# Optimization experiments

Measured on AMD Instinct MI355X. Metric: run time of the kernel, lower is better.

The kernel has to match this reference:

```python
import jax, jax.numpy as jnp
import numpy as np
import math

B, S, H = 8, 1024, 1024
LN_EPS = 1e-5  # assumed epsilon of create_normalization_layer('layer_norm')


def setup_inputs() -> dict:
    key = jax.random.key(0)
    ks = jax.random.split(key, 6)
    context = jax.random.normal(ks[0], (B, S, H), dtype=jnp.float32)
    mask = jnp.ones((B, 1, S), dtype=jnp.int32)
    prior = jax.random.uniform(ks[1], (B, S, S), dtype=jnp.float32)
    # LayerNorm params
    gamma = jnp.ones((H,), dtype=jnp.float32)
    beta = jnp.zeros((H,), dtype=jnp.float32)
    # Dense projections (Glorot-like init)
    scale = 1.0 / np.sqrt(H)
    Wk = jax.random.normal(ks[2], (H, H), dtype=jnp.float32) * scale
    bk = jnp.zeros((H,), dtype=jnp.float32)
    Wq = jax.random.normal(ks[3], (H, H), dtype=jnp.float32) * scale
    bq = jnp.zeros((H,), dtype=jnp.float32)
    return {"context": context, "mask": mask, "prior": prior,
            "gamma": gamma, "beta": beta, "Wk": Wk, "bk": bk, "Wq": Wq, "bq": bq}


def reference(context, mask, prior, gamma, beta, Wk, bk, Wq, bq):
    dtype = context.dtype
    s = context.shape[1]
    hs = context.shape[2]
    i = jnp.arange(s)
    adj_upper = i[:, None] == (i[None, :] - 1)          # [S,S] superdiagonal
    adj_lower = i[:, None] == (i[None, :] + 1)          # subdiagonal
    adj_mask = adj_upper | adj_lower
    pad = mask[:, 0, :].astype(bool)                    # [B,S]
    pad2d = pad[:, :, None] & pad[:, None, :]           # [B,S,S]
    final_adj = adj_mask[None, :, :] & pad2d

    # LayerNorm over last axis
    mu = jnp.mean(context, axis=-1, keepdims=True)
    var = jnp.mean(jnp.square(context - mu), axis=-1, keepdims=True)
    cn = (context - mu) * jax.lax.rsqrt(var + LN_EPS) * gamma + beta

    k = cn @ Wk + bk                                    # [B,S,H]
    q = cn @ Wq + bq
    scores = jnp.einsum('bsh,bth->bst', q, k) / math.sqrt(hs)
    scores = jnp.where(final_adj, scores, jnp.asarray(-1e9, dtype))
    neibor = jax.nn.softmax(scores, axis=-1)
    neibor = jnp.sqrt(neibor * jnp.swapaxes(neibor, 1, 2) + 1e-9)
    neibor = prior + (1.0 - prior) * neibor

    triu = i[None, :] >= i[:, None]                     # [S,S] upper incl diag
    tri = triu.astype(dtype)
    b_eye = jnp.eye(s, dtype=bool)

    t = jnp.log(neibor + 1e-9)
    t = jnp.where(adj_upper[None, :, :], t, jnp.asarray(0.0, dtype))
    t = jnp.einsum('bij,jk->bik', t, tri)               # cumulative over cols
    g = jnp.exp(jnp.einsum('ij,bjk->bik', tri, t))      # hierarchical prefix product
    keep = jnp.logical_not(jnp.logical_xor(triu, b_eye))
    g = jnp.where(keep[None, :, :], g, jnp.asarray(0.0, dtype))
    neibor_diag = jnp.where(b_eye[None, :, :], jnp.asarray(1e-9, dtype), neibor)
    g = g + jnp.swapaxes(g, 1, 2) + neibor_diag
    g = g / (jnp.sum(g, axis=-1, keepdims=True) + 1e-9)

    f2d = pad2d.astype(dtype)
    g = g * f2d
    neibor = neibor * f2d
    return g, neibor
```

## Files before the change

kernel.cpp:

```cpp
#include <hip/hip_runtime.h>
#include <hip/hip_bf16.h>

#define SB 8
#define SS 1024
#define SH 1024
#define LN_EPS 1e-5f

typedef unsigned short u16;
typedef __attribute__((ext_vector_type(8))) short bf16x8;
typedef __attribute__((ext_vector_type(4))) float f32x4;

__device__ __forceinline__ u16 f2bf(float f) {
  __hip_bfloat16 h = __float2bfloat16(f);
  return *reinterpret_cast<u16*>(&h);
}
__device__ __forceinline__ float bf2f(u16 x) {
  unsigned v = ((unsigned)x) << 16;
  return __builtin_bit_cast(float, v);
}
__device__ __forceinline__ ushort4 pack4(float a, float b, float c, float d) {
  ushort4 o;
  o.x = f2bf(a); o.y = f2bf(b); o.z = f2bf(c); o.w = f2bf(d);
  return o;
}

__device__ __forceinline__ void gld16(const void* g, void* l) {
  __builtin_amdgcn_global_load_lds(
      (const __attribute__((address_space(1))) void*)g,
      (__attribute__((address_space(3))) void*)l, 16, 0, 0);
}

#define NPT 256
#define NWB 16
#define LNB0 (NPT + NWB)

__global__ __launch_bounds__(256) void prep_pt(
    const float* __restrict__ x, const float* __restrict__ gamma,
    const float* __restrict__ beta, const float* __restrict__ Wq,
    const float* __restrict__ Wk, const float* __restrict__ bq,
    u16* __restrict__ cnb, u16* __restrict__ PT, float* __restrict__ wkbq,
    float* __restrict__ du, float* __restrict__ dd) {
  __shared__ float p1[4], p2[4];
  __shared__ u16 As[64 * 32];
  __shared__ u16 Bs[64 * 32];
  const int blk = blockIdx.x;
  const int t = threadIdx.x;
  const int wave = t >> 6, lane = t & 63;

  if (blk >= LNB0) {
    const int row = blk - LNB0;
    const float* xr = x + (size_t)row * SH;
    float4 v = *(const float4*)(xr + 4 * t);

    float s = v.x + v.y + v.z + v.w;
#pragma unroll
    for (int off = 32; off > 0; off >>= 1) s += __shfl_down(s, off, 64);
    if (lane == 0) p1[wave] = s;
    __syncthreads();
    const float mu = (p1[0] + p1[1] + p1[2] + p1[3]) * (1.0f / SH);

    float d0 = v.x - mu, d1 = v.y - mu, d2 = v.z - mu, d3 = v.w - mu;
    float ss = d0 * d0 + d1 * d1 + d2 * d2 + d3 * d3;
#pragma unroll
    for (int off = 32; off > 0; off >>= 1) ss += __shfl_down(ss, off, 64);
    if (lane == 0) p2[wave] = ss;
    __syncthreads();
    const float rstd =
        rsqrtf((p2[0] + p2[1] + p2[2] + p2[3]) * (1.0f / SH) + LN_EPS);

    float4 gm = *(const float4*)(gamma + 4 * t);
    float4 bt = *(const float4*)(beta + 4 * t);
    ushort4 o = pack4(d0 * rstd * gm.x + bt.x, d1 * rstd * gm.y + bt.y,
                      d2 * rstd * gm.z + bt.z, d3 * rstd * gm.w + bt.w);
    *(ushort4*)(cnb + (size_t)row * SH + 4 * t) = o;
    if (t == 0) {
      du[row] = 0.f;
      dd[row] = 0.f;
    }
  } else if (blk < NPT) {
    const int m0 = (blk >> 4) * 64;
    const int n0 = (blk & 15) * 64;
    const int wn = wave * 16;
    const int l15 = lane & 15, q = lane >> 4;

    f32x4 acc[4] = {};

    const int srow = t >> 2;
    const int scol = (t & 3) * 8;
    const float* gA = Wk + (size_t)(m0 + srow) * SH + scol;
    const float* gB = Wq + (size_t)(n0 + srow) * SH + scol;
    u16* lA = &As[srow * 32 + scol];
    u16* lB = &Bs[srow * 32 + scol];

    for (int k0 = 0; k0 < SH; k0 += 32) {
      float4 a0 = *(const float4*)(gA + k0);
      float4 a1 = *(const float4*)(gA + k0 + 4);
      float4 b0 = *(const float4*)(gB + k0);
      float4 b1 = *(const float4*)(gB + k0 + 4);
      __syncthreads();
      *(ushort4*)lA = pack4(a0.x, a0.y, a0.z, a0.w);
      *(ushort4*)(lA + 4) = pack4(a1.x, a1.y, a1.z, a1.w);
      *(ushort4*)lB = pack4(b0.x, b0.y, b0.z, b0.w);
      *(ushort4*)(lB + 4) = pack4(b1.x, b1.y, b1.z, b1.w);
      __syncthreads();

      bf16x8 af[4];
#pragma unroll
      for (int fm = 0; fm < 4; ++fm)
        af[fm] = *(const bf16x8*)&As[(fm * 16 + l15) * 32 + q * 8];
      bf16x8 bfr = *(const bf16x8*)&Bs[(wn + l15) * 32 + q * 8];
#pragma unroll
      for (int fm = 0; fm < 4; ++fm)
        acc[fm] = __builtin_amdgcn_mfma_f32_16x16x32_bf16(af[fm], bfr, acc[fm],
                                                          0, 0, 0);
    }

#pragma unroll
    for (int fm = 0; fm < 4; ++fm) {
      const int row0 = m0 + fm * 16 + q * 4;
      const int col = n0 + wn + l15;
#pragma unroll
      for (int r = 0; r < 4; ++r)
        PT[(size_t)(row0 + r) * SH + col] = f2bf(acc[fm][r]);
    }
  } else {
    const int rbase = (blk - NPT) * 64 + wave * 16;
    float4 bv[4];
#pragma unroll
    for (int j = 0; j < 4; ++j)
      bv[j] = *(const float4*)(bq + lane * 16 + 4 * j);
    for (int i = 0; i < 16; ++i) {
      const float* wr = Wk + (size_t)(rbase + i) * SH + lane * 16;
      float s = 0.f;
#pragma unroll
      for (int j = 0; j < 4; ++j) {
        float4 w4 = *(const float4*)(wr + 4 * j);
        s += w4.x * bv[j].x + w4.y * bv[j].y + w4.z * bv[j].z + w4.w * bv[j].w;
      }
#pragma unroll
      for (int off = 32; off > 0; off >>= 1) s += __shfl_down(s, off, 64);
      if (lane == 0) wkbq[rbase + i] = s;
    }
  }
}

#define GK 1024
#define GN 1024
#define BM 128
#define BN 128
#define BK 32

__global__ __launch_bounds__(256) void ugemm_fused(const u16* __restrict__ A,
                                                   const u16* __restrict__ Bt,
                                                   const u16* __restrict__ cnb,
                                                   const float* __restrict__ wkbq,
                                                   float* __restrict__ du,
                                                   float* __restrict__ dd) {
  __shared__ u16 As[BM * BK];
  __shared__ u16 Bs[BN * BK];
  __shared__ u16 cn_s[144 * 128];
  const int tid = threadIdx.x;
  const int m0 = blockIdx.y * BM;
  const int n0 = blockIdx.x * BN;
  const int wave = tid >> 6, lane = tid & 63;
  const int wm = (wave & 1) * 64, wn = (wave >> 1) * 64;
  const int l15 = lane & 15, q = lane >> 4;

  {
    const int lr4 = lane >> 4;
    const int cb = lane & 15;
#pragma unroll
    for (int rd = 0; rd < 9; ++rd) {
      const int rowbase = rd * 16 + wave * 4;
      const int rowi = rowbase + lr4;
      const int sw = (rowi >> 2) & 3;
      int gr = m0 - 1 + rowi;
      gr = max(0, min(SB * SS - 1, gr));
      gld16(cnb + (size_t)gr * SH + n0 + (((cb ^ (sw << 1))) << 3),
            &cn_s[rowbase * 128]);
    }
  }

  f32x4 acc[4][4] = {};

  const int srow = tid >> 2;
  const int scol = 8 * (tid & 3);
  const u16* gA = A + (size_t)(m0 + srow) * GK + scol;
  const u16* gB = Bt + (size_t)(n0 + srow) * GK + scol;
  u16* lA = &As[srow * BK + scol];
  u16* lB = &Bs[srow * BK + scol];

  for (int k0 = 0; k0 < GK; k0 += BK) {
    __syncthreads();
    gld16(gA + k0, lA);
    gld16(gA + (size_t)64 * GK + k0, lA + 64 * BK);
    gld16(gB + k0, lB);
    gld16(gB + (size_t)64 * GK + k0, lB + 64 * BK);
    __syncthreads();

    bf16x8 af[4], bfr[4];
#pragma unroll
    for (int fm = 0; fm < 4; ++fm)
      af[fm] = *(const bf16x8*)&As[(wm + fm * 16 + l15) * BK + q * 8];
#pragma unroll
    for (int fn = 0; fn < 4; ++fn)
      bfr[fn] = *(const bf16x8*)&Bs[(wn + fn * 16 + l15) * BK + q * 8];
#pragma unroll
    for (int fm = 0; fm < 4; ++fm)
#pragma unroll
      for (int fn = 0; fn < 4; ++fn)
        acc[fm][fn] = __builtin_amdgcn_mfma_f32_16x16x32_bf16(
            af[fm], bfr[fn], acc[fm][fn], 0, 0, 0);
  }

  float wb[4];
#pragma unroll
  for (int fn = 0; fn < 4; ++fn) wb[fn] = wkbq[n0 + wn + fn * 16 + l15];

#pragma unroll
  for (int fm = 0; fm < 4; ++fm) {
#pragma unroll
    for (int rr = 0; rr < 4; ++rr) {
      const int lr = wm + fm * 16 + q * 4 + rr;
      const int r = m0 + lr;
      const int sl = r & (SS - 1);
      const int ru = lr + 2;
      const int swu = ((ru >> 2) & 3) << 4;
      const int swd = ((lr >> 2) & 3) << 4;
      const u16* up = &cn_s[ru * 128];
      const u16* dn = &cn_s[lr * 128];
      float sdu = 0.f, sdd = 0.f;
#pragma unroll
      for (int fn = 0; fn < 4; ++fn) {
        const int lc = wn + fn * 16 + l15;
        const float a = acc[fm][fn][rr] + wb[fn];
        sdu += a * bf2f(up[lc ^ swu]);
        sdd += a * bf2f(dn[lc ^ swd]);
      }
      if (sl == SS - 1) sdu = 0.f;
      if (sl == 0) sdd = 0.f;
#pragma unroll
      for (int m = 1; m < 16; m <<= 1) {
        sdu += __shfl_xor(sdu, m, 64);
        sdd += __shfl_xor(sdd, m, 64);
      }
      if (l15 == 0) {
        atomicAdd(&du[r], sdu);
        atomicAdd(&dd[r], sdd);
      }
    }
  }
}

__device__ __forceinline__ void soft2(const float* __restrict__ du,
                                      const float* __restrict__ dd, int x,
                                      float& pu, float& pd) {
  const int sl = x & (SS - 1);
  if (sl == 0) { pu = 1.f; pd = 0.f; }
  else if (sl == SS - 1) { pu = 0.f; pd = 1.f; }
  else {
    const float a = du[x] * 0.03125f;
    const float b = dd[x] * 0.03125f;
    const float m = fmaxf(a, b);
    const float eu = __expf(a - m), ed = __expf(b - m);
    const float inv = 1.f / (eu + ed);
    pu = eu * inv;
    pd = ed * inv;
  }
}

__global__ __launch_bounds__(256) void rows_fused(const float* __restrict__ prior,
                                                  const int* __restrict__ mask,
                                                  const float* __restrict__ du,
                                                  const float* __restrict__ dd,
                                                  float* __restrict__ g_out,
                                                  float* __restrict__ ne_out) {
  const int r = blockIdx.x;
  const int b = r >> 10, i = r & (SS - 1);
  const int t = threadIdx.x;
  const int wave = t >> 6, lane = t & 63;
  const float nbz = 3.1622776601683795e-5f;

  float nb_im1 = nbz, nb_ip1 = nbz;
  if (i >= 1) {
    float pu_m, pd_m, pu_c, pd_c;
    soft2(du, dd, r - 1, pu_m, pd_m);
    soft2(du, dd, r, pu_c, pd_c);
    nb_im1 = sqrtf(pu_m * pd_c + 1e-9f);
  }
  if (i <= SS - 2) {
    float pu_c, pd_c, pu_p, pd_p;
    soft2(du, dd, r, pu_c, pd_c);
    soft2(du, dd, r + 1, pu_p, pd_p);
    nb_ip1 = sqrtf(pu_c * pd_p + 1e-9f);
  }

  const float* prow = prior + (size_t)r * SS;
  float4 pr = *(const float4*)(prow + 4 * t);
  const int* mrow = mask + b * SS;
  const float padi = (mrow[i] != 0) ? 1.f : 0.f;
  int4 mk = *(const int4*)(mrow + 4 * t);

  float ne[4], gsum = 0.f;
#pragma unroll
  for (int v = 0; v < 4; ++v) {
    const int k = 4 * t + v;
    const float p = (&pr.x)[v];
    const float nb = (k == i - 1) ? nb_im1 : (k == i + 1) ? nb_ip1 : nbz;
    const float n = p + (1.f - p) * nb;
    ne[v] = n;
    gsum += (k == i) ? (2.f + 1e-9f) : (1.f + n);
  }

  __shared__ float part[4];
#pragma unroll
  for (int off = 32; off > 0; off >>= 1) gsum += __shfl_down(gsum, off, 64);
  if (lane == 0) part[wave] = gsum;
  __syncthreads();
  const float inv = 1.f / (part[0] + part[1] + part[2] + part[3] + 1e-9f);

  float4 go, no;
#pragma unroll
  for (int v = 0; v < 4; ++v) {
    const int k = 4 * t + v;
    const float padk = ((&mk.x)[v] != 0) ? 1.f : 0.f;
    const float f2 = padi * padk;
    const float gt = (k == i) ? (2.f + 1e-9f) : (1.f + ne[v]);
    (&go.x)[v] = gt * inv * f2;
    (&no.x)[v] = ne[v] * f2;
  }
  *(float4*)(g_out + (size_t)r * SS + 4 * t) = go;
  *(float4*)(ne_out + (size_t)r * SS + 4 * t) = no;
}

extern "C" void kernel_launch(void* const* d_in, const int* in_sizes, int n_in,
                              void* d_out, int out_size, void* d_ws, size_t ws_size,
                              hipStream_t stream) {
  const float* context = (const float*)d_in[0];
  const int* mask = (const int*)d_in[1];
  const float* prior = (const float*)d_in[2];
  const float* gamma = (const float*)d_in[3];
  const float* beta = (const float*)d_in[4];
  const float* Wk = (const float*)d_in[5];
  const float* bk = (const float*)d_in[6];
  const float* Wq = (const float*)d_in[7];
  const float* bq = (const float*)d_in[8];
  (void)bk;

  float* out_g = (float*)d_out;
  float* out_n = out_g + (size_t)SB * SS * SS;

  char* ws = (char*)d_ws;
  u16* cnb = (u16*)ws;
  u16* PT = (u16*)(ws + ((size_t)16 << 20));
  float* wkbq = (float*)(ws + ((size_t)18 << 20));
  float* du = (float*)(ws + ((size_t)19 << 20));
  float* dd = (float*)(ws + ((size_t)20 << 20));

  prep_pt<<<LNB0 + SB * SS, 256, 0, stream>>>(context, gamma, beta, Wq, Wk, bq,
                                              cnb, PT, wkbq, du, dd);
  ugemm_fused<<<dim3(8, 64), 256, 0, stream>>>(cnb, PT, cnb, wkbq, du, dd);
  rows_fused<<<SB * SS, 256, 0, stream>>>(prior, mask, du, dd, out_g, out_n);
}
```

Measured before the change: 191.5 us.

## Merge three kernels into one cooperative persistent kernel with grid syncs

Replaces the prep, GEMM and row-output kernels with a single cooperative kernel of 512 blocks that separates the phases with grid.sync(). LayerNorm rows are spread across all blocks after the small weight GEMM, and the row output phase has each block loop over 16 rows. The aim is to remove launch gaps and tail effects between kernels. In exchange, grid-wide barriers are added, occupancy is capped at two blocks per CU, and the memory-bound final phase runs with far fewer blocks, which may lower bandwidth utilisation.

```diff
diff --git a/kernel.cpp b/kernel.cpp
--- a/kernel.cpp
+++ b/kernel.cpp
@@ -1,11 +1,19 @@
 #include <hip/hip_runtime.h>
 #include <hip/hip_bf16.h>
+#include <hip/hip_cooperative_groups.h>
+
+namespace cg = cooperative_groups;
 
 #define SB 8
 #define SS 1024
 #define SH 1024
 #define LN_EPS 1e-5f
 
+#define GK 1024
+#define BM 128
+#define BN 128
+#define BK 32
+
 typedef unsigned short u16;
 typedef __attribute__((ext_vector_type(8))) short bf16x8;
 typedef __attribute__((ext_vector_type(4))) float f32x4;
@@ -23,233 +31,10 @@
   o.x = f2bf(a); o.y = f2bf(b); o.z = f2bf(c); o.w = f2bf(d);
   return o;
 }
-
 __device__ __forceinline__ void gld16(const void* g, void* l) {
   __builtin_amdgcn_global_load_lds(
       (const __attribute__((address_space(1))) void*)g,
       (__attribute__((address_space(3))) void*)l, 16, 0, 0);
-}
-
-#define NPT 256
-#define NWB 16
-#define LNB0 (NPT + NWB)
-
-__global__ __launch_bounds__(256) void prep_pt(
-    const float* __restrict__ x, const float* __restrict__ gamma,
-    const float* __restrict__ beta, const float* __restrict__ Wq,
-    const float* __restrict__ Wk, const float* __restrict__ bq,
-    u16* __restrict__ cnb, u16* __restrict__ PT, float* __restrict__ wkbq,
-    float* __restrict__ du, float* __restrict__ dd) {
-  __shared__ float p1[4], p2[4];
-  __shared__ u16 As[64 * 32];
-  __shared__ u16 Bs[64 * 32];
-  const int blk = blockIdx.x;
-  const int t = threadIdx.x;
-  const int wave = t >> 6, lane = t & 63;
-
-  if (blk >= LNB0) {
-    const int row = blk - LNB0;
-    const float* xr = x + (size_t)row * SH;
-    float4 v = *(const float4*)(xr + 4 * t);
-
-    float s = v.x + v.y + v.z + v.w;
-#pragma unroll
-    for (int off = 32; off > 0; off >>= 1) s += __shfl_down(s, off, 64);
-    if (lane == 0) p1[wave] = s;
-    __syncthreads();
-    const float mu = (p1[0] + p1[1] + p1[2] + p1[3]) * (1.0f / SH);
-
-    float d0 = v.x - mu, d1 = v.y - mu, d2 = v.z - mu, d3 = v.w - mu;
-    float ss = d0 * d0 + d1 * d1 + d2 * d2 + d3 * d3;
-#pragma unroll
-    for (int off = 32; off > 0; off >>= 1) ss += __shfl_down(ss, off, 64);
-    if (lane == 0) p2[wave] = ss;
-    __syncthreads();
-    const float rstd =
-        rsqrtf((p2[0] + p2[1] + p2[2] + p2[3]) * (1.0f / SH) + LN_EPS);
-
-    float4 gm = *(const float4*)(gamma + 4 * t);
-    float4 bt = *(const float4*)(beta + 4 * t);
-    ushort4 o = pack4(d0 * rstd * gm.x + bt.x, d1 * rstd * gm.y + bt.y,
-                      d2 * rstd * gm.z + bt.z, d3 * rstd * gm.w + bt.w);
-    *(ushort4*)(cnb + (size_t)row * SH + 4 * t) = o;
-    if (t == 0) {
-      du[row] = 0.f;
-      dd[row] = 0.f;
-    }
-  } else if (blk < NPT) {
-    const int m0 = (blk >> 4) * 64;
-    const int n0 = (blk & 15) * 64;
-    const int wn = wave * 16;
-    const int l15 = lane & 15, q = lane >> 4;
-
-    f32x4 acc[4] = {};
-
-    const int srow = t >> 2;
-    const int scol = (t & 3) * 8;
-    const float* gA = Wk + (size_t)(m0 + srow) * SH + scol;
-    const float* gB = Wq + (size_t)(n0 + srow) * SH + scol;
-    u16* lA = &As[srow * 32 + scol];
-    u16* lB = &Bs[srow * 32 + scol];
-
-    for (int k0 = 0; k0 < SH; k0 += 32) {
-      float4 a0 = *(const float4*)(gA + k0);
-      float4 a1 = *(const float4*)(gA + k0 + 4);
-      float4 b0 = *(const float4*)(gB + k0);
-      float4 b1 = *(const float4*)(gB + k0 + 4);
-      __syncthreads();
-      *(ushort4*)lA = pack4(a0.x, a0.y, a0.z, a0.w);
-      *(ushort4*)(lA + 4) = pack4(a1.x, a1.y, a1.z, a1.w);
-      *(ushort4*)lB = pack4(b0.x, b0.y, b0.z, b0.w);
-      *(ushort4*)(lB + 4) = pack4(b1.x, b1.y, b1.z, b1.w);
-      __syncthreads();
-
-      bf16x8 af[4];
-#pragma unroll
-      for (int fm = 0; fm < 4; ++fm)
-        af[fm] = *(const bf16x8*)&As[(fm * 16 + l15) * 32 + q * 8];
-      bf16x8 bfr = *(const bf16x8*)&Bs[(wn + l15) * 32 + q * 8];
-#pragma unroll
-      for (int fm = 0; fm < 4; ++fm)
-        acc[fm] = __builtin_amdgcn_mfma_f32_16x16x32_bf16(af[fm], bfr, acc[fm],
-                                                          0, 0, 0);
-    }
-
-#pragma unroll
-    for (int fm = 0; fm < 4; ++fm) {
-      const int row0 = m0 + fm * 16 + q * 4;
-      const int col = n0 + wn + l15;
-#pragma unroll
-      for (int r = 0; r < 4; ++r)
-        PT[(size_t)(row0 + r) * SH + col] = f2bf(acc[fm][r]);
-    }
-  } else {
-    const int rbase = (blk - NPT) * 64 + wave * 16;
-    float4 bv[4];
-#pragma unroll
-    for (int j = 0; j < 4; ++j)
-      bv[j] = *(const float4*)(bq + lane * 16 + 4 * j);
-    for (int i = 0; i < 16; ++i) {
-      const float* wr = Wk + (size_t)(rbase + i) * SH + lane * 16;
-      float s = 0.f;
-#pragma unroll
-      for (int j = 0; j < 4; ++j) {
-        float4 w4 = *(const float4*)(wr + 4 * j);
-        s += w4.x * bv[j].x + w4.y * bv[j].y + w4.z * bv[j].z + w4.w * bv[j].w;
-      }
-#pragma unroll
-      for (int off = 32; off > 0; off >>= 1) s += __shfl_down(s, off, 64);
-      if (lane == 0) wkbq[rbase + i] = s;
-    }
-  }
-}
-
-#define GK 1024
-#define GN 1024
-#define BM 128
-#define BN 128
-#define BK 32
-
-__global__ __launch_bounds__(256) void ugemm_fused(const u16* __restrict__ A,
-                                                   const u16* __restrict__ Bt,
-                                                   const u16* __restrict__ cnb,
-                                                   const float* __restrict__ wkbq,
-                                                   float* __restrict__ du,
-                                                   float* __restrict__ dd) {
-  __shared__ u16 As[BM * BK];
-  __shared__ u16 Bs[BN * BK];
-  __shared__ u16 cn_s[144 * 128];
-  const int tid = threadIdx.x;
-  const int m0 = blockIdx.y * BM;
-  const int n0 = blockIdx.x * BN;
-  const int wave = tid >> 6, lane = tid & 63;
-  const int wm = (wave & 1) * 64, wn = (wave >> 1) * 64;
-  const int l15 = lane & 15, q = lane >> 4;
-
-  {
-    const int lr4 = lane >> 4;
-    const int cb = lane & 15;
-#pragma unroll
-    for (int rd = 0; rd < 9; ++rd) {
-      const int rowbase = rd * 16 + wave * 4;
-      const int rowi = rowbase + lr4;
-      const int sw = (rowi >> 2) & 3;
-      int gr = m0 - 1 + rowi;
-      gr = max(0, min(SB * SS - 1, gr));
-      gld16(cnb + (size_t)gr * SH + n0 + (((cb ^ (sw << 1))) << 3),
-            &cn_s[rowbase * 128]);
-    }
-  }
-
-  f32x4 acc[4][4] = {};
-
-  const int srow = tid >> 2;
-  const int scol = 8 * (tid & 3);
-  const u16* gA = A + (size_t)(m0 + srow) * GK + scol;
-  const u16* gB = Bt + (size_t)(n0 + srow) * GK + scol;
-  u16* lA = &As[srow * BK + scol];
-  u16* lB = &Bs[srow * BK + scol];
-
-  for (int k0 = 0; k0 < GK; k0 += BK) {
-    __syncthreads();
-    gld16(gA + k0, lA);
-    gld16(gA + (size_t)64 * GK + k0, lA + 64 * BK);
-    gld16(gB + k0, lB);
-    gld16(gB + (size_t)64 * GK + k0, lB + 64 * BK);
-    __syncthreads();
-
-    bf16x8 af[4], bfr[4];
-#pragma unroll
-    for (int fm = 0; fm < 4; ++fm)
-      af[fm] = *(const bf16x8*)&As[(wm + fm * 16 + l15) * BK + q * 8];
-#pragma unroll
-    for (int fn = 0; fn < 4; ++fn)
-      bfr[fn] = *(const bf16x8*)&Bs[(wn + fn * 16 + l15) * BK + q * 8];
-#pragma unroll
-    for (int fm = 0; fm < 4; ++fm)
-#pragma unroll
-      for (int fn = 0; fn < 4; ++fn)
-        acc[fm][fn] = __builtin_amdgcn_mfma_f32_16x16x32_bf16(
-            af[fm], bfr[fn], acc[fm][fn], 0, 0, 0);
-  }
-
-  float wb[4];
-#pragma unroll
-  for (int fn = 0; fn < 4; ++fn) wb[fn] = wkbq[n0 + wn + fn * 16 + l15];
-
-#pragma unroll
-  for (int fm = 0; fm < 4; ++fm) {
-#pragma unroll
-    for (int rr = 0; rr < 4; ++rr) {
-      const int lr = wm + fm * 16 + q * 4 + rr;
-      const int r = m0 + lr;
-      const int sl = r & (SS - 1);
-      const int ru = lr + 2;
-      const int swu = ((ru >> 2) & 3) << 4;
-      const int swd = ((lr >> 2) & 3) << 4;
-      const u16* up = &cn_s[ru * 128];
-      const u16* dn = &cn_s[lr * 128];
-      float sdu = 0.f, sdd = 0.f;
-#pragma unroll
-      for (int fn = 0; fn < 4; ++fn) {
-        const int lc = wn + fn * 16 + l15;
-        const float a = acc[fm][fn][rr] + wb[fn];
-        sdu += a * bf2f(up[lc ^ swu]);
-        sdd += a * bf2f(dn[lc ^ swd]);
-      }
-      if (sl == SS - 1) sdu = 0.f;
-      if (sl == 0) sdd = 0.f;
-#pragma unroll
-      for (int m = 1; m < 16; m <<= 1) {
-        sdu += __shfl_xor(sdu, m, 64);
-        sdd += __shfl_xor(sdd, m, 64);
-      }
-      if (l15 == 0) {
-        atomicAdd(&du[r], sdu);
-        atomicAdd(&dd[r], sdd);
-      }
-    }
-  }
 }
 
 __device__ __forceinline__ void soft2(const float* __restrict__ du,
@@ -269,68 +54,290 @@
   }
 }
 
-__global__ __launch_bounds__(256) void rows_fused(const float* __restrict__ prior,
-                                                  const int* __restrict__ mask,
-                                                  const float* __restrict__ du,
-                                                  const float* __restrict__ dd,
-                                                  float* __restrict__ g_out,
-                                                  float* __restrict__ ne_out) {
-  const int r = blockIdx.x;
-  const int b = r >> 10, i = r & (SS - 1);
-  const int t = threadIdx.x;
-  const int wave = t >> 6, lane = t & 63;
-  const float nbz = 3.1622776601683795e-5f;
-
-  float nb_im1 = nbz, nb_ip1 = nbz;
-  if (i >= 1) {
-    float pu_m, pd_m, pu_c, pd_c;
-    soft2(du, dd, r - 1, pu_m, pd_m);
-    soft2(du, dd, r, pu_c, pd_c);
-    nb_im1 = sqrtf(pu_m * pd_c + 1e-9f);
-  }
-  if (i <= SS - 2) {
-    float pu_c, pd_c, pu_p, pd_p;
-    soft2(du, dd, r, pu_c, pd_c);
-    soft2(du, dd, r + 1, pu_p, pd_p);
-    nb_ip1 = sqrtf(pu_c * pd_p + 1e-9f);
-  }
-
-  const float* prow = prior + (size_t)r * SS;
-  float4 pr = *(const float4*)(prow + 4 * t);
-  const int* mrow = mask + b * SS;
-  const float padi = (mrow[i] != 0) ? 1.f : 0.f;
-  int4 mk = *(const int4*)(mrow + 4 * t);
-
-  float ne[4], gsum = 0.f;
-#pragma unroll
-  for (int v = 0; v < 4; ++v) {
-    const int k = 4 * t + v;
-    const float p = (&pr.x)[v];
-    const float nb = (k == i - 1) ? nb_im1 : (k == i + 1) ? nb_ip1 : nbz;
-    const float n = p + (1.f - p) * nb;
-    ne[v] = n;
-    gsum += (k == i) ? (2.f + 1e-9f) : (1.f + n);
-  }
-
-  __shared__ float part[4];
-#pragma unroll
-  for (int off = 32; off > 0; off >>= 1) gsum += __shfl_down(gsum, off, 64);
-  if (lane == 0) part[wave] = gsum;
-  __syncthreads();
-  const float inv = 1.f / (part[0] + part[1] + part[2] + part[3] + 1e-9f);
-
-  float4 go, no;
-#pragma unroll
-  for (int v = 0; v < 4; ++v) {
-    const int k = 4 * t + v;
-    const float padk = ((&mk.x)[v] != 0) ? 1.f : 0.f;
-    const float f2 = padi * padk;
-    const float gt = (k == i) ? (2.f + 1e-9f) : (1.f + ne[v]);
-    (&go.x)[v] = gt * inv * f2;
-    (&no.x)[v] = ne[v] * f2;
-  }
-  *(float4*)(g_out + (size_t)r * SS + 4 * t) = go;
-  *(float4*)(ne_out + (size_t)r * SS + 4 * t) = no;
+#define AS_OFF 0
+#define BS_OFF 8192
+#define CN_OFF 16384
+#define PR_OFF 53248
+#define SMEM_BYTES 53280
+
+__global__ __launch_bounds__(256, 2) void mega(
+    const float* __restrict__ x, const float* __restrict__ gamma,
+    const float* __restrict__ beta, const float* __restrict__ Wq,
+    const float* __restrict__ Wk, const float* __restrict__ bq,
+    const float* __restrict__ prior, const int* __restrict__ mask,
+    u16* __restrict__ cnb, u16* __restrict__ PT, float* __restrict__ wkbq,
+    float* __restrict__ du, float* __restrict__ dd,
+    float* __restrict__ g_out, float* __restrict__ ne_out) {
+  __shared__ __align__(16) char smem[SMEM_BYTES];
+  u16* As = (u16*)(smem + AS_OFF);
+  u16* Bs = (u16*)(smem + BS_OFF);
+  u16* cn_s = (u16*)(smem + CN_OFF);
+  float* p1 = (float*)(smem + PR_OFF);
+  float* p2 = p1 + 4;
+
+  const int bid = blockIdx.x;
+  const int tid = threadIdx.x;
+  const int wave = tid >> 6, lane = tid & 63;
+  cg::grid_group grid = cg::this_grid();
+
+  if (bid < 256) {
+    const int m0 = (bid >> 4) * 64;
+    const int n0 = (bid & 15) * 64;
+    const int wn = wave * 16;
+    const int l15 = lane & 15, q = lane >> 4;
+    u16* tA = As;
+    u16* tB = As + 2048;
+
+    f32x4 acc[4] = {};
+    const int srow = tid >> 2;
+    const int scol = (tid & 3) * 8;
+    const float* gA = Wk + (size_t)(m0 + srow) * SH + scol;
+    const float* gB = Wq + (size_t)(n0 + srow) * SH + scol;
+    u16* lA = &tA[srow * 32 + scol];
+    u16* lB = &tB[srow * 32 + scol];
+
+    for (int k0 = 0; k0 < SH; k0 += 32) {
+      float4 a0 = *(const float4*)(gA + k0);
+      float4 a1 = *(const float4*)(gA + k0 + 4);
+      float4 b0 = *(const float4*)(gB + k0);
+      float4 b1 = *(const float4*)(gB + k0 + 4);
+      __syncthreads();
+      *(ushort4*)lA = pack4(a0.x, a0.y, a0.z, a0.w);
+      *(ushort4*)(lA + 4) = pack4(a1.x, a1.y, a1.z, a1.w);
+      *(ushort4*)lB = pack4(b0.x, b0.y, b0.z, b0.w);
+      *(ushort4*)(lB + 4) = pack4(b1.x, b1.y, b1.z, b1.w);
+      __syncthreads();
+
+      bf16x8 af[4];
+#pragma unroll
+      for (int fm = 0; fm < 4; ++fm)
+        af[fm] = *(const bf16x8*)&tA[(fm * 16 + l15) * 32 + q * 8];
+      bf16x8 bfr = *(const bf16x8*)&tB[(wn + l15) * 32 + q * 8];
+#pragma unroll
+      for (int fm = 0; fm < 4; ++fm)
+        acc[fm] = __builtin_amdgcn_mfma_f32_16x16x32_bf16(af[fm], bfr, acc[fm],
+                                                          0, 0, 0);
+    }
+    __syncthreads();
+#pragma unroll
+    for (int fm = 0; fm < 4; ++fm) {
+      const int row0 = m0 + fm * 16 + q * 4;
+      const int col = n0 + wn + l15;
+#pragma unroll
+      for (int r = 0; r < 4; ++r)
+        PT[(size_t)(row0 + r) * SH + col] = f2bf(acc[fm][r]);
+    }
+  } else if (bid < 272) {
+    const int rbase = (bid - 256) * 64 + wave * 16;
+    float4 bv[4];
+#pragma unroll
+    for (int j = 0; j < 4; ++j)
+      bv[j] = *(const float4*)(bq + lane * 16 + 4 * j);
+    for (int i = 0; i < 16; ++i) {
+      const float* wr = Wk + (size_t)(rbase + i) * SH + lane * 16;
+      float s = 0.f;
+#pragma unroll
+      for (int j = 0; j < 4; ++j) {
+        float4 w4 = *(const float4*)(wr + 4 * j);
+        s += w4.x * bv[j].x + w4.y * bv[j].y + w4.z * bv[j].z + w4.w * bv[j].w;
+      }
+#pragma unroll
+      for (int off = 32; off > 0; off >>= 1) s += __shfl_down(s, off, 64);
+      if (lane == 0) wkbq[rbase + i] = s;
+    }
+  }
+
+  {
+    int row0, nrows;
+    if (bid < 256) { row0 = bid * 8; nrows = 8; }
+    else { row0 = 2048 + (bid - 256) * 24; nrows = 24; }
+    const float4 gm = *(const float4*)(gamma + 4 * tid);
+    const float4 bt = *(const float4*)(beta + 4 * tid);
+    for (int j = 0; j < nrows; ++j) {
+      const int row = row0 + j;
+      const float* xr = x + (size_t)row * SH;
+      float4 v = *(const float4*)(xr + 4 * tid);
+
+      float s = v.x + v.y + v.z + v.w;
+#pragma unroll
+      for (int off = 32; off > 0; off >>= 1) s += __shfl_down(s, off, 64);
+      if (lane == 0) p1[wave] = s;
+      __syncthreads();
+      const float mu = (p1[0] + p1[1] + p1[2] + p1[3]) * (1.0f / SH);
+
+      float d0 = v.x - mu, d1 = v.y - mu, d2 = v.z - mu, d3 = v.w - mu;
+      float ss = d0 * d0 + d1 * d1 + d2 * d2 + d3 * d3;
+#pragma unroll
+      for (int off = 32; off > 0; off >>= 1) ss += __shfl_down(ss, off, 64);
+      if (lane == 0) p2[wave] = ss;
+      __syncthreads();
+      const float rstd =
+          rsqrtf((p2[0] + p2[1] + p2[2] + p2[3]) * (1.0f / SH) + LN_EPS);
+
+      ushort4 o = pack4(d0 * rstd * gm.x + bt.x, d1 * rstd * gm.y + bt.y,
+                        d2 * rstd * gm.z + bt.z, d3 * rstd * gm.w + bt.w);
+      *(ushort4*)(cnb + (size_t)row * SH + 4 * tid) = o;
+      if (tid == 0) {
+        du[row] = 0.f;
+        dd[row] = 0.f;
+      }
+    }
+  }
+
+  grid.sync();
+
+  {
+    const int bx = bid & 7, by = bid >> 3;
+    const int m0 = by * BM, n0 = bx * BN;
+    const int wm = (wave & 1) * 64, wn = (wave >> 1) * 64;
+    const int l15 = lane & 15, q = lane >> 4;
+
+    {
+      const int lr4 = lane >> 4;
+      const int cb = lane & 15;
+#pragma unroll
+      for (int rd = 0; rd < 9; ++rd) {
+        const int rowbase = rd * 16 + wave * 4;
+        const int rowi = rowbase + lr4;
+        const int sw = (rowi >> 2) & 3;
+        int gr = m0 - 1 + rowi;
+        gr = max(0, min(SB * SS - 1, gr));
+        gld16(cnb + (size_t)gr * SH + n0 + ((cb ^ (sw << 1)) << 3),
+              &cn_s[rowbase * 128]);
+      }
+    }
+
+    f32x4 acc[4][4] = {};
+    const int srow = tid >> 2;
+    const int scol = 8 * (tid & 3);
+    const u16* gA = cnb + (size_t)(m0 + srow) * GK + scol;
+    const u16* gB = PT + (size_t)(n0 + srow) * GK + scol;
+    u16* lA = &As[srow * BK + scol];
+    u16* lB = &Bs[srow * BK + scol];
+
+    for (int k0 = 0; k0 < GK; k0 += BK) {
+      __syncthreads();
+      gld16(gA + k0, lA);
+      gld16(gA + (size_t)64 * GK + k0, lA + 64 * BK);
+      gld16(gB + k0, lB);
+      gld16(gB + (size_t)64 * GK + k0, lB + 64 * BK);
+      __syncthreads();
+
+      bf16x8 af[4], bfr[4];
+#pragma unroll
+      for (int fm = 0; fm < 4; ++fm)
+        af[fm] = *(const bf16x8*)&As[(wm + fm * 16 + l15) * BK + q * 8];
+#pragma unroll
+      for (int fn = 0; fn < 4; ++fn)
+        bfr[fn] = *(const bf16x8*)&Bs[(wn + fn * 16 + l15) * BK + q * 8];
+#pragma unroll
+      for (int fm = 0; fm < 4; ++fm)
+#pragma unroll
+        for (int fn = 0; fn < 4; ++fn)
+          acc[fm][fn] = __builtin_amdgcn_mfma_f32_16x16x32_bf16(
+              af[fm], bfr[fn], acc[fm][fn], 0, 0, 0);
+    }
+
+    float wb[4];
+#pragma unroll
+    for (int fn = 0; fn < 4; ++fn) wb[fn] = wkbq[n0 + wn + fn * 16 + l15];
+
+#pragma unroll
+    for (int fm = 0; fm < 4; ++fm) {
+#pragma unroll
+      for (int rr = 0; rr < 4; ++rr) {
+        const int lr = wm + fm * 16 + q * 4 + rr;
+        const int r = m0 + lr;
+        const int sl = r & (SS - 1);
+        const int ru = lr + 2;
+        const int swu = ((ru >> 2) & 3) << 4;
+        const int swd = ((lr >> 2) & 3) << 4;
+        const u16* up = &cn_s[ru * 128];
+        const u16* dn = &cn_s[lr * 128];
+        float sdu = 0.f, sdd = 0.f;
+#pragma unroll
+        for (int fn = 0; fn < 4; ++fn) {
+          const int lc = wn + fn * 16 + l15;
+          const float a = acc[fm][fn][rr] + wb[fn];
+          sdu += a * bf2f(up[lc ^ swu]);
+          sdd += a * bf2f(dn[lc ^ swd]);
+        }
+        if (sl == SS - 1) sdu = 0.f;
+        if (sl == 0) sdd = 0.f;
+#pragma unroll
+        for (int m = 1; m < 16; m <<= 1) {
+          sdu += __shfl_xor(sdu, m, 64);
+          sdd += __shfl_xor(sdd, m, 64);
+        }
+        if (l15 == 0) {
+          atomicAdd(&du[r], sdu);
+          atomicAdd(&dd[r], sdd);
+        }
+      }
+    }
+  }
+
+  grid.sync();
+
+  {
+    float* part = p1;
+    const float nbz = 3.1622776601683795e-5f;
+    for (int j = 0; j < 16; ++j) {
+      const int r = bid * 16 + j;
+      const int b = r >> 10, i = r & (SS - 1);
+
+      float nb_im1 = nbz, nb_ip1 = nbz;
+      if (i >= 1) {
+        float pu_m, pd_m, pu_c, pd_c;
+        soft2(du, dd, r - 1, pu_m, pd_m);
+        soft2(du, dd, r, pu_c, pd_c);
+        nb_im1 = sqrtf(pu_m * pd_c + 1e-9f);
+      }
+      if (i <= SS - 2) {
+        float pu_c, pd_c, pu_p, pd_p;
+        soft2(du, dd, r, pu_c, pd_c);
+        soft2(du, dd, r + 1, pu_p, pd_p);
+        nb_ip1 = sqrtf(pu_c * pd_p + 1e-9f);
+      }
+
+      const float* prow = prior + (size_t)r * SS;
+      float4 pv = *(const float4*)(prow + 4 * tid);
+      const int* mrow = mask + b * SS;
+      const float padi = (mrow[i] != 0) ? 1.f : 0.f;
+      int4 mk = *(const int4*)(mrow + 4 * tid);
+
+      float ne[4], gsum = 0.f;
+#pragma unroll
+      for (int v = 0; v < 4; ++v) {
+        const int k = 4 * tid + v;
+        const float p = (&pv.x)[v];
+        const float nb = (k == i - 1) ? nb_im1 : (k == i + 1) ? nb_ip1 : nbz;
+        const float n = p + (1.f - p) * nb;
+        ne[v] = n;
+        gsum += (k == i) ? (2.f + 1e-9f) : (1.f + n);
+      }
+
+#pragma unroll
+      for (int off = 32; off > 0; off >>= 1) gsum += __shfl_down(gsum, off, 64);
+      if (lane == 0) part[wave] = gsum;
+      __syncthreads();
+      const float inv = 1.f / (part[0] + part[1] + part[2] + part[3] + 1e-9f);
+      __syncthreads();
+
+      float4 go, no;
+#pragma unroll
+      for (int v = 0; v < 4; ++v) {
+        const int k = 4 * tid + v;
+        const float padk = ((&mk.x)[v] != 0) ? 1.f : 0.f;
+        const float f2 = padi * padk;
+        const float gt = (k == i) ? (2.f + 1e-9f) : (1.f + ne[v]);
+        (&go.x)[v] = gt * inv * f2;
+        (&no.x)[v] = ne[v] * f2;
+      }
+      *(float4*)(g_out + (size_t)r * SS + 4 * tid) = go;
+      *(float4*)(ne_out + (size_t)r * SS + 4 * tid) = no;
+    }
+  }
 }
 
 extern "C" void kernel_launch(void* const* d_in, const int* in_sizes, int n_in,
@@ -357,8 +364,10 @@
   float* du = (float*)(ws + ((size_t)19 << 20));
   float* dd = (float*)(ws + ((size_t)20 << 20));
 
-  prep_pt<<<LNB0 + SB * SS, 256, 0, stream>>>(context, gamma, beta, Wq, Wk, bq,
-                                              cnb, PT, wkbq, du, dd);
-  ugemm_fused<<<dim3(8, 64), 256, 0, stream>>>(cnb, PT, cnb, wkbq, du, dd);
-  rows_fused<<<SB * SS, 256, 0, stream>>>(prior, mask, du, dd, out_g, out_n);
-}
+  void* kargs[] = {(void*)&context, (void*)&gamma, (void*)&beta, (void*)&Wq,
+                   (void*)&Wk,      (void*)&bq,    (void*)&prior, (void*)&mask,
+                   (void*)&cnb,     (void*)&PT,    (void*)&wkbq,  (void*)&du,
+                   (void*)&dd,      (void*)&out_g, (void*)&out_n};
+  hipLaunchCooperativeKernel((void*)mega, dim3(512), dim3(256), kargs, 0,
+                             stream);
+}
```

New measurement: 361.5 us. 88.8% more time.

## Double-buffer GEMM LDS tiles and swizzle block order in fused GEMM

Applied to the files above, without the earlier changes.

Converts the ugemm_fused main loop to double-buffered LDS, issuing the next K-tile's global-to-LDS loads before computing on the current tile. Partial vmcnt waits and raw s_barrier replace the two __syncthreads per iteration. It also switches to a 1D grid with a block-index swizzle so consecutive blocks share B tiles, which should improve cache locality. This doubles LDS use for the A/B tiles, which may lower occupancy, and the hand-written waitcnt relies on the loads being counted in the expected order.

```diff
diff --git a/kernel.cpp b/kernel.cpp
--- a/kernel.cpp
+++ b/kernel.cpp
@@ -23,7 +23,6 @@
   o.x = f2bf(a); o.y = f2bf(b); o.z = f2bf(c); o.w = f2bf(d);
   return o;
 }
-
 __device__ __forceinline__ void gld16(const void* g, void* l) {
   __builtin_amdgcn_global_load_lds(
       (const __attribute__((address_space(1))) void*)g,
@@ -84,7 +83,6 @@
     const int l15 = lane & 15, q = lane >> 4;
 
     f32x4 acc[4] = {};
-
     const int srow = t >> 2;
     const int scol = (t & 3) * 8;
     const float* gA = Wk + (size_t)(m0 + srow) * SH + scol;
@@ -145,7 +143,6 @@
 }
 
 #define GK 1024
-#define GN 1024
 #define BM 128
 #define BN 128
 #define BK 32
@@ -156,12 +153,13 @@
                                                    const float* __restrict__ wkbq,
                                                    float* __restrict__ du,
                                                    float* __restrict__ dd) {
-  __shared__ u16 As[BM * BK];
-  __shared__ u16 Bs[BN * BK];
+  __shared__ u16 As[2][BM * BK];
+  __shared__ u16 Bs[2][BN * BK];
   __shared__ u16 cn_s[144 * 128];
   const int tid = threadIdx.x;
-  const int m0 = blockIdx.y * BM;
-  const int n0 = blockIdx.x * BN;
+  const int swz = (blockIdx.x & 7) * 64 + (blockIdx.x >> 3);
+  const int m0 = (swz >> 3) * BM;
+  const int n0 = (swz & 7) * BN;
   const int wave = tid >> 6, lane = tid & 63;
   const int wm = (wave & 1) * 64, wn = (wave >> 1) * 64;
   const int l15 = lane & 15, q = lane >> 4;
@@ -176,35 +174,73 @@
       const int sw = (rowi >> 2) & 3;
       int gr = m0 - 1 + rowi;
       gr = max(0, min(SB * SS - 1, gr));
-      gld16(cnb + (size_t)gr * SH + n0 + (((cb ^ (sw << 1))) << 3),
+      gld16(cnb + (size_t)gr * SH + n0 + ((cb ^ (sw << 1)) << 3),
             &cn_s[rowbase * 128]);
     }
   }
 
   f32x4 acc[4][4] = {};
-
   const int srow = tid >> 2;
   const int scol = 8 * (tid & 3);
   const u16* gA = A + (size_t)(m0 + srow) * GK + scol;
   const u16* gB = Bt + (size_t)(n0 + srow) * GK + scol;
-  u16* lA = &As[srow * BK + scol];
-  u16* lB = &Bs[srow * BK + scol];
-
-  for (int k0 = 0; k0 < GK; k0 += BK) {
-    __syncthreads();
-    gld16(gA + k0, lA);
-    gld16(gA + (size_t)64 * GK + k0, lA + 64 * BK);
-    gld16(gB + k0, lB);
-    gld16(gB + (size_t)64 * GK + k0, lB + 64 * BK);
-    __syncthreads();
-
+  const int so = srow * BK + scol;
+
+  gld16(gA, &As[0][so]);
+  gld16(gA + (size_t)64 * GK, &As[0][64 * BK + so]);
+  gld16(gB, &Bs[0][so]);
+  gld16(gB + (size_t)64 * GK, &Bs[0][64 * BK + so]);
+
+  int cur = 0;
+  for (int t = 0; t < 31; ++t) {
+    const int k1 = (t + 1) * BK;
+    u16* nA = &As[cur ^ 1][so];
+    u16* nB = &Bs[cur ^ 1][so];
+    gld16(gA + k1, nA);
+    gld16(gA + (size_t)64 * GK + k1, nA + 64 * BK);
+    gld16(gB + k1, nB);
+    gld16(gB + (size_t)64 * GK + k1, nB + 64 * BK);
+
+    asm volatile("s_waitcnt vmcnt(4)" ::: "memory");
+    __builtin_amdgcn_sched_barrier(0);
+    __builtin_amdgcn_s_barrier();
+    __builtin_amdgcn_sched_barrier(0);
+
+    const u16* cA = As[cur];
+    const u16* cB = Bs[cur];
     bf16x8 af[4], bfr[4];
 #pragma unroll
     for (int fm = 0; fm < 4; ++fm)
-      af[fm] = *(const bf16x8*)&As[(wm + fm * 16 + l15) * BK + q * 8];
+      af[fm] = *(const bf16x8*)&cA[(wm + fm * 16 + l15) * BK + q * 8];
 #pragma unroll
     for (int fn = 0; fn < 4; ++fn)
-      bfr[fn] = *(const bf16x8*)&Bs[(wn + fn * 16 + l15) * BK + q * 8];
+      bfr[fn] = *(const bf16x8*)&cB[(wn + fn * 16 + l15) * BK + q * 8];
+#pragma unroll
+    for (int fm = 0; fm < 4; ++fm)
+#pragma unroll
+      for (int fn = 0; fn < 4; ++fn)
+        acc[fm][fn] = __builtin_amdgcn_mfma_f32_16x16x32_bf16(
+            af[fm], bfr[fn], acc[fm][fn], 0, 0, 0);
+
+    __builtin_amdgcn_s_barrier();
+    __builtin_amdgcn_sched_barrier(0);
+    cur ^= 1;
+  }
+
+  asm volatile("s_waitcnt vmcnt(0)" ::: "memory");
+  __builtin_amdgcn_sched_barrier(0);
+  __builtin_amdgcn_s_barrier();
+  __builtin_amdgcn_sched_barrier(0);
+  {
+    const u16* cA = As[cur];
+    const u16* cB = Bs[cur];
+    bf16x8 af[4], bfr[4];
+#pragma unroll
+    for (int fm = 0; fm < 4; ++fm)
+      af[fm] = *(const bf16x8*)&cA[(wm + fm * 16 + l15) * BK + q * 8];
+#pragma unroll
+    for (int fn = 0; fn < 4; ++fn)
+      bfr[fn] = *(const bf16x8*)&cB[(wn + fn * 16 + l15) * BK + q * 8];
 #pragma unroll
     for (int fm = 0; fm < 4; ++fm)
 #pragma unroll
@@ -359,6 +395,6 @@
 
   prep_pt<<<LNB0 + SB * SS, 256, 0, stream>>>(context, gamma, beta, Wq, Wk, bq,
                                               cnb, PT, wkbq, du, dd);
-  ugemm_fused<<<dim3(8, 64), 256, 0, stream>>>(cnb, PT, cnb, wkbq, du, dd);
+  ugemm_fused<<<512, 256, 0, stream>>>(cnb, PT, cnb, wkbq, du, dd);
   rows_fused<<<SB * SS, 256, 0, stream>>>(prior, mask, du, dd, out_g, out_n);
 }
```

Result: no change. 189.9 us, median of 2 (-0.8%).
